# Optimization experiments

Hardware: AMD Instinct MI355X
Metric: run time of the kernel (lower is better)

Reference implementation:

```python
import jax, jax.numpy as jnp
import numpy as np

B, N, D, NH, T = 4, 1024, 512, 8, 2
H = D // NH  # attention_head_size = 64
NTYPES = 8


def setup_inputs() -> dict:
    key = jax.random.key(0)
    ks = jax.random.split(key, 16)
    w = lambda k, s: jax.random.normal(k, s, jnp.float32) * 0.05
    inp = {
        'node_embedding': jax.random.normal(ks[0], (B, N, D), jnp.float32),
        'question_embedding': jax.random.normal(ks[1], (B, 1, D), jnp.float32),
        'W_fc_w': w(ks[2], (D, 2 * D)),
        'w_dc_w': w(ks[3], (T, 2 * D, D)),
        'dense_w': w(ks[4], (2 * D, 2 * D)),
        'ln_in_g': jnp.ones((2 * D,), jnp.float32), 'ln_in_b': jnp.zeros((2 * D,), jnp.float32),
        'W_qv_w': w(ks[5], (2 * D, D)), 'W_kv_w': w(ks[6], (2 * D, D)), 'W_vv_w': w(ks[7], (2 * D, D)),
        'W_qc_w': w(ks[8], (D, D)), 'W_kc_w': w(ks[9], (D, D)), 'W_vc_w': w(ks[10], (D, D)),
        'ln_q_g': jnp.ones((D,), jnp.float32), 'ln_q_b': jnp.zeros((D,), jnp.float32),
        'ln_k_g': jnp.ones((D,), jnp.float32), 'ln_k_b': jnp.zeros((D,), jnp.float32),
        'ln_v_g': jnp.ones((D,), jnp.float32), 'ln_v_b': jnp.zeros((D,), jnp.float32),
        'W_att': w(ks[11], (1 + NTYPES, 2 * H)),  # row 0 = entity-number, rows 1..8 = number types
        'W_u_w': w(ks[12], (2 * D, D)),
        'ln_out_g': jnp.ones((D,), jnp.float32), 'ln_out_b': jnp.zeros((D,), jnp.float32),
    }
    # masks must be disjoint (assert max(sum of masks) <= 1): partition a categorical
    r = jax.random.randint(ks[13], (B, N, N), 0, NTYPES + 2)
    inp['mask_entity'] = (r == 0).astype(jnp.int32)
    inp['mask_types'] = jnp.stack([(r == k + 1).astype(jnp.int32) for k in range(NTYPES)], 0)
    return inp


def _ln(x, g, b):
    m = jnp.mean(x, -1, keepdims=True)
    v = jnp.mean(jnp.square(x - m), -1, keepdims=True)
    return (x - m) * jax.lax.rsqrt(v + 1e-12) * g + b


def _forward(node_embedding, question_embedding, W_fc_w, w_dc_w, dense_w, ln_in_g, ln_in_b,
             W_qv_w, W_kv_w, W_vv_w, W_qc_w, W_kc_w, W_vc_w,
             ln_q_g, ln_q_b, ln_k_g, ln_k_b, ln_v_g, ln_v_b,
             W_att, W_u_w, ln_out_g, ln_out_b, mask_entity, mask_types):
    node_enc = node_embedding
    # eval mode: dropout is identity
    for t in range(T):
        m_t = jax.nn.elu(question_embedding @ W_fc_w) @ w_dc_w[t]  # [B,1,D]
        ie = jnp.concatenate([node_enc, node_embedding], -1) @ dense_w  # [B,N,2D]
        ie = _ln(ie, ln_in_g, ln_in_b)
        # qd=True: question-directed gating
        xq = _ln((ie @ W_qv_w) * (m_t @ W_qc_w), ln_q_g, ln_q_b)
        xk = _ln((ie @ W_kv_w) * (m_t @ W_kc_w), ln_k_g, ln_k_b)
        xv = _ln((ie @ W_vv_w) * (m_t @ W_vc_w), ln_v_g, ln_v_b)
        split = lambda x: x.reshape(B, N, NH, H).transpose(0, 2, 1, 3)  # [B,H,N,h]
        xq, xk, xv = split(xq), split(xk), split(xv)
        # additive attention W([q_i; k_j]) == q_i.Wq + k_j.Wk : compute rank-1 parts, no NxN concat
        a_src = jnp.einsum('bhnd,md->mbhn', xq, W_att[:, :H])  # [9,B,H,N]
        a_dst = jnp.einsum('bhnd,md->mbhn', xk, W_att[:, H:])
        score = jnp.where(mask_entity[:, None, :, :] > 0,
                          a_src[0][..., :, None] + a_dst[0][..., None, :], 0.0)
        for k in range(NTYPES):
            score = score + jnp.where(mask_types[k][:, None, :, :] > 0,
                                      a_src[k + 1][..., :, None] + a_dst[k + 1][..., None, :], 0.0)
        score = jnp.where(score > 0, score, 0.01 * score)  # F.leaky_relu default slope
        mask_total = (mask_entity + jnp.sum(mask_types, 0))[:, None, :, :].astype(score.dtype)  # [B,1,N,N]
        # allennlp masked_softmax (default branch)
        p = jax.nn.softmax(score * mask_total, axis=-1) * mask_total
        p = p / (jnp.sum(p, -1, keepdims=True) + 1e-13)
        p = jnp.where(mask_total > 0, p, 0.0)
        X = jnp.einsum('bhij,bhjd->bhid', p, xv).transpose(0, 2, 1, 3).reshape(B, N, D)
        node_enc = _ln(jnp.concatenate([node_enc, X], -1) @ W_u_w, ln_out_g, ln_out_b)
    return node_enc


def reference(node_embedding, question_embedding, W_fc_w, w_dc_w, dense_w, ln_in_g, ln_in_b,
              W_qv_w, W_kv_w, W_vv_w, W_qc_w, W_kc_w, W_vc_w,
              ln_q_g, ln_q_b, ln_k_g, ln_k_b, ln_v_g, ln_v_b,
              W_att, W_u_w, ln_out_g, ln_out_b, mask_entity, mask_types):
    return _forward(node_embedding, question_embedding, W_fc_w, w_dc_w, dense_w, ln_in_g, ln_in_b,
                    W_qv_w, W_kv_w, W_vv_w, W_qc_w, W_kc_w, W_vc_w,
                    ln_q_g, ln_q_b, ln_k_g, ln_k_b, ln_v_g, ln_v_b,
                    W_att, W_u_w, ln_out_g, ln_out_b, mask_entity, mask_types)
```

## Files before the change

kernel.cpp:

```cpp
#include <hip/hip_runtime.h>
#include <stdint.h>

typedef unsigned short u16;
typedef short v8s __attribute__((ext_vector_type(8)));
typedef float v4f __attribute__((ext_vector_type(4)));

__device__ __forceinline__ float bf2f(u16 u) {
  union { unsigned int i; float f; } v; v.i = ((unsigned int)u) << 16; return v.f;
}
__device__ __forceinline__ u16 f2bf(float f) {
  union { float f; unsigned int i; } v; v.f = f;
  unsigned int r = v.i + 0x7FFFu + ((v.i >> 16) & 1u);
  return (u16)(r >> 16);
}
__device__ __forceinline__ int probe_f32(const void* p) {
  return ((const u16*)p)[0] != 0x3F80;
}

#define GLOAD16(g, l) __builtin_amdgcn_global_load_lds( \
    (__attribute__((address_space(1))) void*)(g), \
    (__attribute__((address_space(3))) void*)(l), 16, 0, 0)

__launch_bounds__(256)
__global__ void setup_cat(const int4* __restrict__ me,
                          const int4* __restrict__ mt,
                          uchar4* __restrict__ cat) {
  const int base = (blockIdx.x << 10) + threadIdx.x;
  int4 a0 = me[base], a1 = me[base + 256], a2 = me[base + 512], a3 = me[base + 768];
  int c[4][4];
  c[0][0]=a0.x; c[0][1]=a0.y; c[0][2]=a0.z; c[0][3]=a0.w;
  c[1][0]=a1.x; c[1][1]=a1.y; c[1][2]=a1.z; c[1][3]=a1.w;
  c[2][0]=a2.x; c[2][1]=a2.y; c[2][2]=a2.z; c[2][3]=a2.w;
  c[3][0]=a3.x; c[3][1]=a3.y; c[3][2]=a3.z; c[3][3]=a3.w;
  #pragma unroll
  for (int k = 0; k < 8; k++) {
    const int4* mk = mt + ((size_t)k << 20);
    int4 m0 = mk[base], m1 = mk[base + 256], m2 = mk[base + 512], m3 = mk[base + 768];
    const int w = k + 2;
    c[0][0]+=w*m0.x; c[0][1]+=w*m0.y; c[0][2]+=w*m0.z; c[0][3]+=w*m0.w;
    c[1][0]+=w*m1.x; c[1][1]+=w*m1.y; c[1][2]+=w*m1.z; c[1][3]+=w*m1.w;
    c[2][0]+=w*m2.x; c[2][1]+=w*m2.y; c[2][2]+=w*m2.z; c[2][3]+=w*m2.w;
    c[3][0]+=w*m3.x; c[3][1]+=w*m3.y; c[3][2]+=w*m3.z; c[3][3]+=w*m3.w;
  }
  #pragma unroll
  for (int j = 0; j < 4; j++) {
    uchar4 o;
    o.x=(unsigned char)c[j][0]; o.y=(unsigned char)c[j][1];
    o.z=(unsigned char)c[j][2]; o.w=(unsigned char)c[j][3];
    cat[base + j * 256] = o;
  }
}

struct SetupTab {
  const void* csrc[12]; void* cdst[12]; int cn4[12]; int cblk[12];
  const void* tsrc[5];
  u16* dwT; u16* wqkvT;
  const void* probe;
};

__device__ void tr_body(const void* src, u16* dst, int R, int C, int r0, int c0,
                        int f32, u16 (*t)[65]) {
  const int tx = threadIdx.x & 63, ty = threadIdx.x >> 6;
  #pragma unroll
  for (int i = 0; i < 16; i++) {
    int r = (i << 2) + ty;
    size_t off = (size_t)(r0 + r) * C + c0 + tx;
    t[r][tx] = f32 ? f2bf(((const float*)src)[off]) : ((const u16*)src)[off];
  }
  __syncthreads();
  #pragma unroll
  for (int i = 0; i < 16; i++) {
    int c = (i << 2) + ty;
    dst[(size_t)(c0 + c) * R + r0 + tx] = t[tx][c];
  }
}

__launch_bounds__(256)
__global__ void setup_all(SetupTab tab) {
  __shared__ u16 t[64][65];
  const int blk = blockIdx.x, tid = threadIdx.x;
  const int f32 = probe_f32(tab.probe);
  if (blk < 715) {
    int rel = blk, tt = 0;
    while (rel >= tab.cblk[tt]) { rel -= tab.cblk[tt]; tt++; }
    const int n4 = tab.cn4[tt], stride = tab.cblk[tt] << 8;
    const float4* sf = (const float4*)tab.csrc[tt];
    const ushort4* sb = (const ushort4*)tab.csrc[tt];
    ushort4* d = (ushort4*)tab.cdst[tt];
    for (int i = (rel << 8) + tid; i < n4; i += stride) {
      ushort4 o;
      if (f32) { float4 v = sf[i]; o.x=f2bf(v.x); o.y=f2bf(v.y); o.z=f2bf(v.z); o.w=f2bf(v.w); }
      else o = sb[i];
      d[i] = o;
    }
  } else if (blk < 971) {
    const int idx = blk - 715;
    tr_body(tab.tsrc[0], tab.dwT, 1024, 1024, (idx >> 4) << 6, (idx & 15) << 6, f32, t);
  } else {
    const int idx = blk - 971;
    const int tt = idx >> 7, rem = idx & 127;
    tr_body(tab.tsrc[1 + tt], tab.wqkvT + (size_t)tt * 524288,
            1024, 512, (rem >> 3) << 6, (rem & 7) << 6, f32, t);
  }
}

template<int BM, int NJ, int MODE>
__launch_bounds__(256, 2)
__global__ void gemm_p(const u16* __restrict__ A0, int lda0,
                       const u16* __restrict__ A1, int lda1, int ksplit,
                       const u16* __restrict__ Bm, int ldb,
                       float* __restrict__ Cf, int ldc, int K,
                       const float* __restrict__ gate) {
  constexpr int WR = (BM == 128) ? 2 : 1;
  constexpr int WC = 4 / WR;
  constexpr int BN = WC * NJ * 16;
  constexpr int RA = BM / 64, RB = BN / 64, R = RA + RB;
  constexpr int TSZ = (BM + BN) * 32;
  __shared__ u16 lds[4 * TSZ];
  const int tid = threadIdx.x;
  const int wid = tid >> 6, lane = tid & 63;
  const int wr = (WR == 2) ? (wid >> 1) : 0;
  const int wc = (WR == 2) ? (wid & 1) : wid;
  const int lm = lane & 15, quad = lane >> 4;
  const int m0 = blockIdx.x * BM, n0 = blockIdx.y * BN;
  const int srow = tid >> 2;
  const int kcol = (tid & 3) << 3;

  auto stage = [&](int buf, int k0) {
    u16* Ad = lds + buf * TSZ;
    u16* Bd = Ad + BM * 32;
    const int kg = k0 + kcol;
    #pragma unroll
    for (int p = 0; p < RA; p++) {
      const int row = m0 + (p << 6) + srow;
      const u16* s = (kg < ksplit) ? (A0 + (size_t)row * lda0 + kg)
                                   : (A1 + (size_t)row * lda1 + (kg - ksplit));
      GLOAD16(s, &Ad[(p << 11) + (wid << 9)]);
    }
    #pragma unroll
    for (int p = 0; p < RB; p++) {
      GLOAD16(Bm + (size_t)(n0 + (p << 6) + srow) * ldb + kg,
              &Bd[(p << 11) + (wid << 9)]);
    }
  };

  v4f acc[4][NJ];
  #pragma unroll
  for (int i = 0; i < 4; i++)
    #pragma unroll
    for (int j = 0; j < NJ; j++) acc[i][j] = v4f{0.f,0.f,0.f,0.f};

  const int S = K >> 5;
  stage(0, 0);
  int issued = 1;
  if (S > 1) { stage(1, 32); issued = 2; }

  for (int s = 0; s < S; s++) {
    if (issued < S) { stage(issued & 3, issued << 5); issued++; }
    const int fly = issued - s;
    if (fly >= 3) {
      asm volatile("s_waitcnt vmcnt(%0)" :: "n"(2 * R) : "memory");
    } else if (fly == 2) {
      asm volatile("s_waitcnt vmcnt(%0)" :: "n"(R) : "memory");
    } else {
      asm volatile("s_waitcnt vmcnt(0)" ::: "memory");
    }
    __builtin_amdgcn_s_barrier();
    __builtin_amdgcn_sched_barrier(0);
    const u16* Ab = lds + (s & 3) * TSZ;
    const u16* Bb = Ab + BM * 32;
    v8s af[4], bfr[NJ];
    #pragma unroll
    for (int i = 0; i < 4; i++)
      af[i] = *(const v8s*)&Ab[(wr*64 + i*16 + lm)*32 + quad*8];
    #pragma unroll
    for (int j = 0; j < NJ; j++)
      bfr[j] = *(const v8s*)&Bb[(wc*(NJ*16) + j*16 + lm)*32 + quad*8];
    #pragma unroll
    for (int i = 0; i < 4; i++)
      #pragma unroll
      for (int j = 0; j < NJ; j++)
        acc[i][j] = __builtin_amdgcn_mfma_f32_16x16x32_bf16(af[i], bfr[j], acc[i][j], 0, 0, 0);
  }

  #pragma unroll
  for (int i = 0; i < 4; i++) {
    #pragma unroll
    for (int j = 0; j < NJ; j++) {
      int col = n0 + wc*(NJ*16) + j*16 + lm;
      #pragma unroll
      for (int r = 0; r < 4; r++) {
        int row = m0 + wr*64 + i*16 + quad*4 + r;
        float v = acc[i][j][r];
        if (MODE == 0) {
          Cf[(size_t)row * ldc + col] = v;
        } else {
          float g = gate[(((col >> 9) << 2) + (row >> 10)) * 512 + (col & 511)];
          Cf[(size_t)row * ldc + col] = v * g;
        }
      }
    }
  }
}

__launch_bounds__(256)
__global__ void gates_a(const void* __restrict__ q, const void* __restrict__ Wfc,
                        float* __restrict__ t1, const void* probe) {
  __shared__ float qs[2048];
  __shared__ float part[4][4][64];
  const int tid = threadIdx.x;
  const int f32 = probe_f32(probe);
  for (int i = tid; i < 2048; i += 256)
    qs[i] = f32 ? ((const float*)q)[i] : bf2f(((const u16*)q)[i]);
  __syncthreads();
  const int col = (blockIdx.x << 6) + (tid & 63);
  const int kq = tid >> 6;
  float a0 = 0, a1 = 0, a2 = 0, a3 = 0;
  if (f32) {
    const float* W = (const float*)Wfc;
    for (int kk = 0; kk < 128; kk++) {
      int k = kq * 128 + kk;
      float w = W[(size_t)k * 1024 + col];
      a0 += qs[k]*w; a1 += qs[512+k]*w; a2 += qs[1024+k]*w; a3 += qs[1536+k]*w;
    }
  } else {
    const u16* W = (const u16*)Wfc;
    for (int kk = 0; kk < 128; kk++) {
      int k = kq * 128 + kk;
      float w = bf2f(W[(size_t)k * 1024 + col]);
      a0 += qs[k]*w; a1 += qs[512+k]*w; a2 += qs[1024+k]*w; a3 += qs[1536+k]*w;
    }
  }
  part[kq][0][tid&63]=a0; part[kq][1][tid&63]=a1;
  part[kq][2][tid&63]=a2; part[kq][3][tid&63]=a3;
  __syncthreads();
  const int b = tid >> 6, c = tid & 63;
  float s = part[0][b][c]+part[1][b][c]+part[2][b][c]+part[3][b][c];
  s = s > 0.f ? s : __expf(s) - 1.0f;
  t1[(b << 10) + (blockIdx.x << 6) + c] = s;
}

__launch_bounds__(256)
__global__ void gates_b(const float* __restrict__ t1, const void* __restrict__ wdc,
                        float* __restrict__ mt, const void* probe) {
  __shared__ float ts[4096];
  __shared__ float part[4][4][64];
  const int tid = threadIdx.x;
  const int f32 = probe_f32(probe);
  for (int i = tid; i < 4096; i += 256) ts[i] = t1[i];
  __syncthreads();
  const int t = blockIdx.y;
  const int col = (blockIdx.x << 6) + (tid & 63);
  const int kq = tid >> 6;
  float a0 = 0, a1 = 0, a2 = 0, a3 = 0;
  if (f32) {
    const float* W = (const float*)wdc;
    for (int kk = 0; kk < 256; kk++) {
      int k = kq * 256 + kk;
      float w = W[((size_t)(t << 10) + k) * 512 + col];
      a0 += ts[k]*w; a1 += ts[1024+k]*w; a2 += ts[2048+k]*w; a3 += ts[3072+k]*w;
    }
  } else {
    const u16* W = (const u16*)wdc;
    for (int kk = 0; kk < 256; kk++) {
      int k = kq * 256 + kk;
      float w = bf2f(W[((size_t)(t << 10) + k) * 512 + col]);
      a0 += ts[k]*w; a1 += ts[1024+k]*w; a2 += ts[2048+k]*w; a3 += ts[3072+k]*w;
    }
  }
  part[kq][0][tid&63]=a0; part[kq][1][tid&63]=a1;
  part[kq][2][tid&63]=a2; part[kq][3][tid&63]=a3;
  __syncthreads();
  const int b = tid >> 6, c = tid & 63;
  float s = part[0][b][c]+part[1][b][c]+part[2][b][c]+part[3][b][c];
  mt[((t * 4 + b) << 9) + (blockIdx.x << 6) + c] = s;
}

__launch_bounds__(256)
__global__ void gates_c(const float* __restrict__ mt,
                        const void* __restrict__ Wqc, const void* __restrict__ Wkc,
                        const void* __restrict__ Wvc, float* __restrict__ gates,
                        const void* probe) {
  __shared__ float ms[2048];
  __shared__ float part[4][4][64];
  const int tid = threadIdx.x;
  const int f32 = probe_f32(probe);
  const int s_ = blockIdx.y, t = blockIdx.z;
  for (int i = tid; i < 2048; i += 256) ms[i] = mt[(t << 11) + i];
  __syncthreads();
  const void* W = (s_ == 0) ? Wqc : ((s_ == 1) ? Wkc : Wvc);
  const int col = (blockIdx.x << 6) + (tid & 63);
  const int kq = tid >> 6;
  float a0 = 0, a1 = 0, a2 = 0, a3 = 0;
  if (f32) {
    const float* Wf = (const float*)W;
    for (int kk = 0; kk < 128; kk++) {
      int k = kq * 128 + kk;
      float w = Wf[(size_t)k * 512 + col];
      a0 += ms[k]*w; a1 += ms[512+k]*w; a2 += ms[1024+k]*w; a3 += ms[1536+k]*w;
    }
  } else {
    const u16* Wb = (const u16*)W;
    for (int kk = 0; kk < 128; kk++) {
      int k = kq * 128 + kk;
      float w = bf2f(Wb[(size_t)k * 512 + col]);
      a0 += ms[k]*w; a1 += ms[512+k]*w; a2 += ms[1024+k]*w; a3 += ms[1536+k]*w;
    }
  }
  part[kq][0][tid&63]=a0; part[kq][1][tid&63]=a1;
  part[kq][2][tid&63]=a2; part[kq][3][tid&63]=a3;
  __syncthreads();
  const int b = tid >> 6, c = tid & 63;
  float s = part[0][b][c]+part[1][b][c]+part[2][b][c]+part[3][b][c];
  gates[(((t * 3 + s_) * 4 + b) << 9) + (blockIdx.x << 6) + c] = s;
}

template<int NE>
__launch_bounds__(256)
__global__ void ln_rows(const float* __restrict__ src, int sstride, int ssegoff,
                        void* __restrict__ dst, int dstride, int dsegoff,
                        int finalout, const void* probe,
                        const u16* __restrict__ g0, const u16* __restrict__ b0,
                        const u16* __restrict__ g1, const u16* __restrict__ b1,
                        const u16* __restrict__ g2, const u16* __restrict__ b2) {
  constexpr int W = NE * 256;
  const int row = blockIdx.x, seg = blockIdx.y;
  const u16* g  = (seg == 0) ? g0 : ((seg == 1) ? g1 : g2);
  const u16* bb = (seg == 0) ? b0 : ((seg == 1) ? b1 : b2);
  const float* x = src + (size_t)row * sstride + (size_t)seg * ssegoff;
  const size_t dbase = (size_t)row * dstride + (size_t)seg * dsegoff;
  const int f32out = finalout ? probe_f32(probe) : 0;
  const int tid = threadIdx.x;
  const int wid = tid >> 6, lane = tid & 63;
  __shared__ float red[4];
  float v[NE];
  float s = 0.f;
  #pragma unroll
  for (int i = 0; i < NE; i++) { v[i] = x[tid + (i << 8)]; s += v[i]; }
  #pragma unroll
  for (int off = 32; off; off >>= 1) s += __shfl_xor(s, off, 64);
  if (lane == 0) red[wid] = s;
  __syncthreads();
  float mean = (red[0]+red[1]+red[2]+red[3]) * (1.0f / W);
  float q = 0.f;
  #pragma unroll
  for (int i = 0; i < NE; i++) { float dd = v[i] - mean; q += dd * dd; }
  __syncthreads();
  #pragma unroll
  for (int off = 32; off; off >>= 1) q += __shfl_xor(q, off, 64);
  if (lane == 0) red[wid] = q;
  __syncthreads();
  float var = (red[0]+red[1]+red[2]+red[3]) * (1.0f / W);
  float rs = rsqrtf(var + 1e-12f);
  #pragma unroll
  for (int i = 0; i < NE; i++) {
    int c = tid + (i << 8);
    float y = (v[i] - mean) * rs * bf2f(g[c]) + bf2f(bb[c]);
    if (f32out) ((float*)dst)[dbase + c] = y;
    else        ((u16*)dst)[dbase + c] = f2bf(y);
  }
}

__launch_bounds__(256)
__global__ void proj_and_xvt(const u16* __restrict__ xqkv, const u16* __restrict__ Watt,
                             float* __restrict__ asrc, float* __restrict__ adst,
                             u16* __restrict__ xvT) {
  __shared__ char shraw[8320];
  const int blk = blockIdx.x, tid = threadIdx.x;
  if (blk >= 1024) {
    const int idx = blk - 1024;
    const int z = idx >> 7, rem = idx & 127;
    tr_body(xqkv + 2ull*4096*512 + (size_t)z * 524288, xvT + (size_t)z * 524288,
            1024, 512, (rem >> 3) << 6, (rem & 7) << 6, 0, (u16(*)[65])shraw);
    return;
  }
  float (*w)[128] = (float(*)[128])shraw;
  for (int i = tid; i < 9 * 128; i += 256) w[i / 128][i % 128] = bf2f(Watt[i]);
  __syncthreads();
  const int wid = tid >> 6, lane = tid & 63;
  const int row = blk * 4 + wid;
  const int b = row >> 10, n = row & 1023;
  const u16* xq = xqkv;
  const u16* xk = xqkv + 4096ull*512;
  v8s q8 = *(const v8s*)&xq[(size_t)row * 512 + lane * 8];
  v8s k8 = *(const v8s*)&xk[(size_t)row * 512 + lane * 8];
  float qf[8], kf[8];
  #pragma unroll
  for (int j = 0; j < 8; j++) { qf[j] = bf2f((u16)q8[j]); kf[j] = bf2f((u16)k8[j]); }
  const int h = lane >> 3, lh = lane & 7;
  #pragma unroll
  for (int m = 0; m < 9; m++) {
    float ps = 0.f, pd = 0.f;
    #pragma unroll
    for (int j = 0; j < 8; j++) {
      ps += qf[j] * w[m][lh * 8 + j];
      pd += kf[j] * w[m][64 + lh * 8 + j];
    }
    #pragma unroll
    for (int off = 1; off < 8; off <<= 1) {
      ps += __shfl_xor(ps, off, 64);
      pd += __shfl_xor(pd, off, 64);
    }
    if (lh == 0) {
      size_t base = (size_t)(b * 8 + h) * 9216 + n * 9 + m;
      asrc[base] = ps;
      adst[base] = pd;
    }
  }
}

__launch_bounds__(512, 4)
__global__ void attn_pv(const unsigned char* __restrict__ cat,
                        const float* __restrict__ asrc,
                        const float* __restrict__ adst,
                        const u16* __restrict__ xvT,
                        u16* __restrict__ xcat) {
  const int bh = blockIdx.y;
  const int b = bh >> 3, h = bh & 7;
  const int it = blockIdx.x, i0 = it << 6;
  __shared__ __align__(16) float adst_s[9216];
  __shared__ __align__(16) u16 P_lds[2][16 * 520];
  __shared__ float asrc_s[576];
  __shared__ __align__(16) float accbuf[16][68];
  __shared__ float psum_lds[2][16];
  const int tid = threadIdx.x;
  const float* ad = adst + (size_t)bh * 9216;
  for (int i = tid; i < 9216; i += 512) adst_s[i] = ad[i];
  const float* as = asrc + (size_t)bh * 9216 + (size_t)i0 * 9;
  for (int i = tid; i < 576; i += 512) asrc_s[i] = as[i];
  __syncthreads();
  const int wid = tid >> 6, lane = tid & 63;
  const int half = wid >> 2, wl = wid & 3;
  const int joff = half << 9;
  const int lm = lane & 15, quad = lane >> 4;
  const float* adh = adst_s + half * 4608;
  u16* Ph = P_lds[half];

  for (int ph = 0; ph < 4; ph++) {
    if (ph) __syncthreads();
    #pragma unroll
    for (int rr = 0; rr < 4; rr++) {
      const int lr = wl * 4 + rr;
      const int r  = ph * 16 + lr;
      const u16* crow = (const u16*)(cat + (((size_t)(b << 10) + i0 + r) << 10) + joff);
      float sum = 0.f;
      #pragma unroll
      for (int s = 0; s < 4; s++) {
        const int j0 = s * 128 + lane * 2;
        unsigned int cc2 = crow[s * 64 + lane];
        float z0 = 0.f, z1 = 0.f;
        int c0 = cc2 & 255, c1 = (cc2 >> 8) & 255;
        if (c0) {
          float sc = asrc_s[r * 9 + c0 - 1] + adh[j0 * 9 + c0 - 1];
          z0 = __expf(sc > 0.f ? sc : 0.01f * sc);
        }
        if (c1) {
          float sc = asrc_s[r * 9 + c1 - 1] + adh[(j0 + 1) * 9 + c1 - 1];
          z1 = __expf(sc > 0.f ? sc : 0.01f * sc);
        }
        sum += z0 + z1;
        unsigned int pk = (unsigned int)f2bf(z0) | ((unsigned int)f2bf(z1) << 16);
        ((unsigned int*)Ph)[(lr * 520 + j0) >> 1] = pk;
      }
      #pragma unroll
      for (int off = 32; off; off >>= 1) sum += __shfl_xor(sum, off, 64);
      if (lane == 0) psum_lds[half][lr] = sum;
    }
    __syncthreads();
    v4f ac0 = v4f{0.f,0.f,0.f,0.f}, ac1 = v4f{0.f,0.f,0.f,0.f};
    v4f ac2 = v4f{0.f,0.f,0.f,0.f}, ac3 = v4f{0.f,0.f,0.f,0.f};
    const u16* xvc = xvT + ((size_t)(bh << 6) + (wl * 16 + lm)) * 1024 + joff;
    #pragma unroll
    for (int c = 0; c < 16; c += 4) {
      v8s a0 = *(const v8s*)&Ph[lm * 520 + (c+0) * 32 + quad * 8];
      v8s b0 = *(const v8s*)&xvc[(c+0) * 32 + quad * 8];
      ac0 = __builtin_amdgcn_mfma_f32_16x16x32_bf16(a0, b0, ac0, 0, 0, 0);
      v8s a1 = *(const v8s*)&Ph[lm * 520 + (c+1) * 32 + quad * 8];
      v8s b1 = *(const v8s*)&xvc[(c+1) * 32 + quad * 8];
      ac1 = __builtin_amdgcn_mfma_f32_16x16x32_bf16(a1, b1, ac1, 0, 0, 0);
      v8s a2 = *(const v8s*)&Ph[lm * 520 + (c+2) * 32 + quad * 8];
      v8s b2 = *(const v8s*)&xvc[(c+2) * 32 + quad * 8];
      ac2 = __builtin_amdgcn_mfma_f32_16x16x32_bf16(a2, b2, ac2, 0, 0, 0);
      v8s a3 = *(const v8s*)&Ph[lm * 520 + (c+3) * 32 + quad * 8];
      v8s b3 = *(const v8s*)&xvc[(c+3) * 32 + quad * 8];
      ac3 = __builtin_amdgcn_mfma_f32_16x16x32_bf16(a3, b3, ac3, 0, 0, 0);
    }
    v4f acc = (ac0 + ac1) + (ac2 + ac3);
    if (half == 0) {
      #pragma unroll
      for (int r = 0; r < 4; r++)
        accbuf[quad * 4 + r][wl * 16 + lm] = acc[r];
    }
    __syncthreads();
    if (half == 1) {
      #pragma unroll
      for (int r = 0; r < 4; r++) {
        const int lrow = quad * 4 + r;
        const float inv = 1.0f / (psum_lds[0][lrow] + psum_lds[1][lrow] + 1e-13f);
        const float v = (accbuf[lrow][wl * 16 + lm] + acc[r]) * inv;
        const int grow = i0 + ph * 16 + lrow;
        xcat[(((size_t)(b << 10) + grow) << 9) + (h << 6) + wl * 16 + lm] = f2bf(v);
      }
    }
  }
}

extern "C" void kernel_launch(void* const* d_in, const int* in_sizes, int n_in,
                              void* d_out, int out_size, void* d_ws, size_t ws_size,
                              hipStream_t stream) {
  char* wptr = (char*)d_ws;
  auto alloc = [&](size_t bytes) {
    char* p = wptr; wptr += (bytes + 255) & ~(size_t)255; return p;
  };
  uint8_t* cat   = (uint8_t*)alloc(4ull << 20);
  u16* dwT       = (u16*)alloc(1024ull*1024*2);
  u16* wqkvT     = (u16*)alloc(2048ull*1024*2);
  u16* wuT       = wqkvT + 1536*1024;
  float* gates   = (float*)alloc(2ull*3*4*512*4);
  float* t1buf   = (float*)alloc(4096ull*4);
  float* mtbuf   = (float*)alloc(4096ull*4);
  u16* c_node    = (u16*)alloc(2097152ull*2);
  u16* c_small   = (u16*)alloc(16384ull*2);
  float* ie_pre  = (float*)alloc(4096ull*1024*4);
  float* qkv_pre = (float*)alloc(4096ull*1536*4);
  u16* ie        = (u16*)alloc(4096ull*1024*2);
  u16* xqkv      = (u16*)alloc(3ull*4096*512*2);
  float* asrc    = (float*)alloc(32ull*9216*4);
  float* adst    = (float*)alloc(32ull*9216*4);
  u16* xvT       = (u16*)alloc(32ull*64*1024*2);
  u16* xcat      = (u16*)alloc(4096ull*512*2);
  float* u_pre   = (float*)alloc(4096ull*512*4);
  u16* node_enc  = (u16*)alloc(4096ull*512*2);

  const void* probe = d_in[5];

  static const int sidx[11] = {5, 6, 13, 14, 15, 16, 17, 18, 19, 21, 22};
  static const int ssz[11]  = {1024, 1024, 512, 512, 512, 512, 512, 512, 1152, 512, 512};
  u16* sp[11]; int off = 0;
  for (int i = 0; i < 11; i++) { sp[i] = c_small + off; off += (ssz[i] + 127) & ~127; }
  const u16 *c_lin_g = sp[0], *c_lin_b = sp[1];
  const u16 *c_lq_g = sp[2], *c_lq_b = sp[3];
  const u16 *c_lk_g = sp[4], *c_lk_b = sp[5];
  const u16 *c_lv_g = sp[6], *c_lv_b = sp[7];
  const u16 *c_Watt = sp[8];
  const u16 *c_lo_g = sp[9], *c_lo_b = sp[10];

  SetupTab tab;
  tab.csrc[0] = d_in[0]; tab.cdst[0] = c_node; tab.cn4[0] = 2097152/4; tab.cblk[0] = 704;
  for (int i = 0; i < 11; i++) {
    tab.csrc[1+i] = d_in[sidx[i]]; tab.cdst[1+i] = sp[i];
    tab.cn4[1+i] = ssz[i] / 4; tab.cblk[1+i] = 1;
  }
  tab.tsrc[0] = d_in[4];
  tab.tsrc[1] = d_in[7];
  tab.tsrc[2] = d_in[8];
  tab.tsrc[3] = d_in[9];
  tab.tsrc[4] = d_in[20];
  tab.dwT = dwT; tab.wqkvT = wqkvT;
  tab.probe = probe;

  setup_cat<<<1024, 256, 0, stream>>>((const int4*)d_in[23], (const int4*)d_in[24],
                                      (uchar4*)cat);
  setup_all<<<1483, 256, 0, stream>>>(tab);
  gates_a<<<16, 256, 0, stream>>>(d_in[1], d_in[2], t1buf, probe);
  gates_b<<<dim3(8,2), 256, 0, stream>>>(t1buf, d_in[3], mtbuf, probe);
  gates_c<<<dim3(8,3,2), 256, 0, stream>>>(mtbuf, d_in[10], d_in[11], d_in[12],
                                           gates, probe);

  const u16* ne_cur = c_node;
  for (int t = 0; t < 2; ++t) {
    gemm_p<128,4,0><<<dim3(32,8), 256, 0, stream>>>(
        ne_cur, 512, c_node, 512, 512, dwT, 1024, ie_pre, 1024, 1024, nullptr);
    ln_rows<4><<<dim3(4096,1), 256, 0, stream>>>(
        ie_pre, 1024, 0, ie, 1024, 0, 0, probe,
        c_lin_g, c_lin_b, c_lin_g, c_lin_b, c_lin_g, c_lin_b);
    gemm_p<128,4,1><<<dim3(32,12), 256, 0, stream>>>(
        ie, 1024, ie, 1024, 1024, wqkvT, 1024, qkv_pre, 1536, 1024, gates + t*6144);
    ln_rows<2><<<dim3(4096,3), 256, 0, stream>>>(
        qkv_pre, 1536, 512, xqkv, 512, 4096*512, 0, probe,
        c_lq_g, c_lq_b, c_lk_g, c_lk_b, c_lv_g, c_lv_b);
    proj_and_xvt<<<1536, 256, 0, stream>>>(xqkv, c_Watt, asrc, adst, xvT);
    attn_pv<<<dim3(16,32), 512, 0, stream>>>(cat, asrc, adst, xvT, xcat);
    gemm_p<64,2,0><<<dim3(64,4), 256, 0, stream>>>(
        ne_cur, 512, xcat, 512, 512, wuT, 1024, u_pre, 512, 1024, nullptr);
    void* dst = (t == 1) ? d_out : (void*)node_enc;
    ln_rows<2><<<dim3(4096,1), 256, 0, stream>>>(
        u_pre, 512, 0, dst, 512, 0, (t == 1) ? 1 : 0, probe,
        c_lo_g, c_lo_b, c_lo_g, c_lo_b, c_lo_g, c_lo_b);
    ne_cur = node_enc;
  }
  (void)in_sizes; (void)n_in; (void)out_size; (void)ws_size;
}
```

Baseline: 581.6 us.

## Split-K the gate GEMVs across more blocks with atomic accumulation

```diff
diff --git a/kernel.cpp b/kernel.cpp
--- a/kernel.cpp
+++ b/kernel.cpp
@@ -55,6 +55,7 @@
   const void* csrc[12]; void* cdst[12]; int cn4[12]; int cblk[12];
   const void* tsrc[5];
   u16* dwT; u16* wqkvT;
+  float* zbuf;
   const void* probe;
 };
 
@@ -96,11 +97,14 @@
   } else if (blk < 971) {
     const int idx = blk - 715;
     tr_body(tab.tsrc[0], tab.dwT, 1024, 1024, (idx >> 4) << 6, (idx & 15) << 6, f32, t);
-  } else {
+  } else if (blk < 1483) {
     const int idx = blk - 971;
     const int tt = idx >> 7, rem = idx & 127;
     tr_body(tab.tsrc[1 + tt], tab.wqkvT + (size_t)tt * 524288,
             1024, 512, (rem >> 3) << 6, (rem & 7) << 6, f32, t);
+  } else {
+    const int idx = blk - 1483;
+    ((float4*)tab.zbuf)[(idx << 8) + tid] = float4{0.f, 0.f, 0.f, 0.f};
   }
 }
 
@@ -206,29 +210,34 @@
 __launch_bounds__(256)
 __global__ void gates_a(const void* __restrict__ q, const void* __restrict__ Wfc,
                         float* __restrict__ t1, const void* probe) {
-  __shared__ float qs[2048];
+  __shared__ float qs[256];
   __shared__ float part[4][4][64];
   const int tid = threadIdx.x;
   const int f32 = probe_f32(probe);
-  for (int i = tid; i < 2048; i += 256)
-    qs[i] = f32 ? ((const float*)q)[i] : bf2f(((const u16*)q)[i]);
+  const int kg = blockIdx.y << 6;
+  {
+    const int b = tid >> 6, kk = tid & 63;
+    const int k = kg + kk;
+    qs[tid] = f32 ? ((const float*)q)[(b << 9) + k]
+                  : bf2f(((const u16*)q)[(b << 9) + k]);
+  }
   __syncthreads();
   const int col = (blockIdx.x << 6) + (tid & 63);
   const int kq = tid >> 6;
   float a0 = 0, a1 = 0, a2 = 0, a3 = 0;
   if (f32) {
     const float* W = (const float*)Wfc;
-    for (int kk = 0; kk < 128; kk++) {
-      int k = kq * 128 + kk;
-      float w = W[(size_t)k * 1024 + col];
-      a0 += qs[k]*w; a1 += qs[512+k]*w; a2 += qs[1024+k]*w; a3 += qs[1536+k]*w;
+    for (int kk = 0; kk < 16; kk++) {
+      int kl = kq * 16 + kk;
+      float w = W[(size_t)(kg + kl) * 1024 + col];
+      a0 += qs[kl]*w; a1 += qs[64+kl]*w; a2 += qs[128+kl]*w; a3 += qs[192+kl]*w;
     }
   } else {
     const u16* W = (const u16*)Wfc;
-    for (int kk = 0; kk < 128; kk++) {
-      int k = kq * 128 + kk;
-      float w = bf2f(W[(size_t)k * 1024 + col]);
-      a0 += qs[k]*w; a1 += qs[512+k]*w; a2 += qs[1024+k]*w; a3 += qs[1536+k]*w;
+    for (int kk = 0; kk < 16; kk++) {
+      int kl = kq * 16 + kk;
+      float w = bf2f(W[(size_t)(kg + kl) * 1024 + col]);
+      a0 += qs[kl]*w; a1 += qs[64+kl]*w; a2 += qs[128+kl]*w; a3 += qs[192+kl]*w;
     }
   }
   part[kq][0][tid&63]=a0; part[kq][1][tid&63]=a1;
@@ -236,36 +245,40 @@
   __syncthreads();
   const int b = tid >> 6, c = tid & 63;
   float s = part[0][b][c]+part[1][b][c]+part[2][b][c]+part[3][b][c];
-  s = s > 0.f ? s : __expf(s) - 1.0f;
-  t1[(b << 10) + (blockIdx.x << 6) + c] = s;
+  atomicAdd(&t1[(b << 10) + (blockIdx.x << 6) + c], s);
 }
 
 __launch_bounds__(256)
 __global__ void gates_b(const float* __restrict__ t1, const void* __restrict__ wdc,
                         float* __restrict__ mt, const void* probe) {
-  __shared__ float ts[4096];
+  __shared__ float ts[1024];
   __shared__ float part[4][4][64];
   const int tid = threadIdx.x;
   const int f32 = probe_f32(probe);
-  for (int i = tid; i < 4096; i += 256) ts[i] = t1[i];
-  __syncthreads();
-  const int t = blockIdx.y;
+  const int kg = blockIdx.y << 8;
+  const int t = blockIdx.z;
+  for (int i = tid; i < 1024; i += 256) {
+    const int b = i >> 8, kk = i & 255;
+    float v = t1[(b << 10) + kg + kk];
+    ts[i] = v > 0.f ? v : __expf(v) - 1.0f;
+  }
+  __syncthreads();
   const int col = (blockIdx.x << 6) + (tid & 63);
   const int kq = tid >> 6;
   float a0 = 0, a1 = 0, a2 = 0, a3 = 0;
   if (f32) {
     const float* W = (const float*)wdc;
-    for (int kk = 0; kk < 256; kk++) {
-      int k = kq * 256 + kk;
-      float w = W[((size_t)(t << 10) + k) * 512 + col];
-      a0 += ts[k]*w; a1 += ts[1024+k]*w; a2 += ts[2048+k]*w; a3 += ts[3072+k]*w;
+    for (int kk = 0; kk < 64; kk++) {
+      int kl = kq * 64 + kk;
+      float w = W[((size_t)(t << 10) + kg + kl) * 512 + col];
+      a0 += ts[kl]*w; a1 += ts[256+kl]*w; a2 += ts[512+kl]*w; a3 += ts[768+kl]*w;
     }
   } else {
     const u16* W = (const u16*)wdc;
-    for (int kk = 0; kk < 256; kk++) {
-      int k = kq * 256 + kk;
-      float w = bf2f(W[((size_t)(t << 10) + k) * 512 + col]);
-      a0 += ts[k]*w; a1 += ts[1024+k]*w; a2 += ts[2048+k]*w; a3 += ts[3072+k]*w;
+    for (int kk = 0; kk < 64; kk++) {
+      int kl = kq * 64 + kk;
+      float w = bf2f(W[((size_t)(t << 10) + kg + kl) * 512 + col]);
+      a0 += ts[kl]*w; a1 += ts[256+kl]*w; a2 += ts[512+kl]*w; a3 += ts[768+kl]*w;
     }
   }
   part[kq][0][tid&63]=a0; part[kq][1][tid&63]=a1;
@@ -273,7 +286,7 @@
   __syncthreads();
   const int b = tid >> 6, c = tid & 63;
   float s = part[0][b][c]+part[1][b][c]+part[2][b][c]+part[3][b][c];
-  mt[((t * 4 + b) << 9) + (blockIdx.x << 6) + c] = s;
+  atomicAdd(&mt[((t * 4 + b) << 9) + (blockIdx.x << 6) + c], s);
 }
 
 __launch_bounds__(256)
@@ -557,13 +570,14 @@
   tab.tsrc[3] = d_in[9];
   tab.tsrc[4] = d_in[20];
   tab.dwT = dwT; tab.wqkvT = wqkvT;
+  tab.zbuf = t1buf;
   tab.probe = probe;
 
   setup_cat<<<1024, 256, 0, stream>>>((const int4*)d_in[23], (const int4*)d_in[24],
                                       (uchar4*)cat);
-  setup_all<<<1483, 256, 0, stream>>>(tab);
-  gates_a<<<16, 256, 0, stream>>>(d_in[1], d_in[2], t1buf, probe);
-  gates_b<<<dim3(8,2), 256, 0, stream>>>(t1buf, d_in[3], mtbuf, probe);
+  setup_all<<<1491, 256, 0, stream>>>(tab);
+  gates_a<<<dim3(16,8), 256, 0, stream>>>(d_in[1], d_in[2], t1buf, probe);
+  gates_b<<<dim3(8,4,2), 256, 0, stream>>>(t1buf, d_in[3], mtbuf, probe);
   gates_c<<<dim3(8,3,2), 256, 0, stream>>>(mtbuf, d_in[10], d_in[11], d_in[12],
                                            gates, probe);
 
```

Result: faster. 558.4 us (-4.0%).
